# Kernel tuning notes

Measured on AMD Instinct MI355X. Metric: run time of the kernel, lower is better.

Reference implementation:

```python
import jax, jax.numpy as jnp
import numpy as np

N = 50000
E = 800000
G = 8
IN, HID, OUT = 128, 256, 128
BN_EPS = 1e-5


def _linear_params(key, fan_in, fan_out):
    k1, k2 = jax.random.split(key)
    s = 1.0 / np.sqrt(fan_in)
    w = jax.random.uniform(k1, (fan_out, fan_in), jnp.float32, -s, s)
    b = jax.random.uniform(k2, (fan_out,), jnp.float32, -s, s)
    return w, b


def setup_inputs() -> dict:
    key = jax.random.key(0)
    ks = jax.random.split(key, 16)
    inp = {
        "x": jax.random.normal(ks[0], (N, IN), jnp.float32),
        "src": jax.random.randint(ks[1], (E,), 0, N, jnp.int32),
        "dst": jax.random.randint(ks[2], (E,), 0, N, jnp.int32),
        "graph_ids": jnp.sort(jax.random.randint(ks[3], (N,), 0, G, jnp.int32)),
    }
    dims = [(IN, HID, HID), (HID, HID, HID), (HID, OUT, OUT)]
    for i, (d_in, d_mid, d_out) in enumerate(dims):
        kk = jax.random.split(ks[4 + i], 2)
        w1, b1 = _linear_params(kk[0], d_in, d_mid)
        w2, b2 = _linear_params(kk[1], d_mid, d_out)
        inp[f"w1_{i}"] = w1
        inp[f"b1_{i}"] = b1
        inp[f"w2_{i}"] = w2
        inp[f"b2_{i}"] = b2
        inp[f"eps_{i}"] = jnp.zeros((), jnp.float32)          # learn_eps, init 0
        inp[f"gamma_{i}"] = jnp.ones((d_out,), jnp.float32)   # BatchNorm weight
        inp[f"beta_{i}"] = jnp.zeros((d_out,), jnp.float32)   # BatchNorm bias
    return inp


def _gin_layer(h, src, dst, w1, b1, w2, b2, eps, gamma, beta):
    # GINConv: (1 + eps) * h_v + sum_{u in N(v)} h_u   (copy_u / sum)
    agg = jax.ops.segment_sum(h[src], dst, num_segments=N)
    z = (1.0 + eps) * h + agg
    # 2-layer MLP with ReLU
    z = jnp.maximum(z @ w1.T + b1, 0.0) @ w2.T + b2
    # BatchNorm1d (training-mode batch statistics, biased variance)
    mu = jnp.mean(z, axis=0)
    var = jnp.var(z, axis=0)
    return (z - mu) * jax.lax.rsqrt(var + BN_EPS) * gamma + beta


def reference(x, src, dst, graph_ids,
              w1_0, b1_0, w2_0, b2_0, eps_0, gamma_0, beta_0,
              w1_1, b1_1, w2_1, b2_1, eps_1, gamma_1, beta_1,
              w1_2, b1_2, w2_2, b2_2, eps_2, gamma_2, beta_2):
    h = _gin_layer(x, src, dst, w1_0, b1_0, w2_0, b2_0, eps_0, gamma_0, beta_0)
    h = jnp.maximum(h, 0.0)  # relu (dropout = identity in eval)
    h = _gin_layer(h, src, dst, w1_1, b1_1, w2_1, b2_1, eps_1, gamma_1, beta_1)
    h = jnp.maximum(h, 0.0)
    h = _gin_layer(h, src, dst, w1_2, b1_2, w2_2, b2_2, eps_2, gamma_2, beta_2)
    # dgl.mean_nodes: per-graph mean over nodes -> [G, OUT]
    sums = jax.ops.segment_sum(h, graph_ids, num_segments=G)
    counts = jax.ops.segment_sum(jnp.ones((N,), h.dtype), graph_ids, num_segments=G)
    return sums / jnp.maximum(counts, 1.0)[:, None]
```

## Files before the change

kernel.cpp:

```cpp
#include <hip/hip_runtime.h>

#define NG 8

typedef _Float16 half8  __attribute__((ext_vector_type(8)));
typedef float    f32x16 __attribute__((ext_vector_type(16)));


__global__ __launch_bounds__(256)
void k_cast16(const float* __restrict__ in, _Float16* __restrict__ out, int n8) {
    int i = blockIdx.x * 256 + threadIdx.x;
    if (i < n8) {
        const float4 a = *(const float4*)(in + (size_t)i * 8);
        const float4 b = *(const float4*)(in + (size_t)i * 8 + 4);
        half8 o;
        o[0] = (_Float16)a.x; o[1] = (_Float16)a.y; o[2] = (_Float16)a.z; o[3] = (_Float16)a.w;
        o[4] = (_Float16)b.x; o[5] = (_Float16)b.y; o[6] = (_Float16)b.z; o[7] = (_Float16)b.w;
        *(half8*)(out + (size_t)i * 8) = o;
    }
}

__global__ __launch_bounds__(256)
void k_castw(const float* __restrict__ w0, const float* __restrict__ w1,
             const float* __restrict__ w2, const float* __restrict__ w3,
             const float* __restrict__ w4, const float* __restrict__ w5,
             _Float16* __restrict__ o0, _Float16* __restrict__ o1,
             _Float16* __restrict__ o2, _Float16* __restrict__ o3,
             _Float16* __restrict__ o4, _Float16* __restrict__ o5) {
    int i = blockIdx.x * 256 + threadIdx.x;
    const float* in; _Float16* out; int off;
    if      (i <  4096) { in = w0; out = o0; off = 0;     }
    else if (i < 12288) { in = w1; out = o1; off = 4096;  }
    else if (i < 20480) { in = w2; out = o2; off = 12288; }
    else if (i < 28672) { in = w3; out = o3; off = 20480; }
    else if (i < 32768) { in = w4; out = o4; off = 28672; }
    else if (i < 34816) { in = w5; out = o5; off = 32768; }
    else return;
    int j = i - off;
    const float4 a = *(const float4*)(in + (size_t)j * 8);
    const float4 b = *(const float4*)(in + (size_t)j * 8 + 4);
    half8 o;
    o[0] = (_Float16)a.x; o[1] = (_Float16)a.y; o[2] = (_Float16)a.z; o[3] = (_Float16)a.w;
    o[4] = (_Float16)b.x; o[5] = (_Float16)b.y; o[6] = (_Float16)b.z; o[7] = (_Float16)b.w;
    *(half8*)(out + (size_t)j * 8) = o;
}


__global__ __launch_bounds__(256)
void k_deg(const int* __restrict__ dst, int* __restrict__ deg, int E) {
    int i = blockIdx.x * 256 + threadIdx.x;
    if (i < E) atomicAdd(&deg[dst[i]], 1);
}

__global__ __launch_bounds__(1024)
void k_scan_a(const int* __restrict__ deg, int* __restrict__ incl,
              int* __restrict__ bsum, int n) {
    __shared__ int s[1024];
    int t = threadIdx.x;
    int base = blockIdx.x * 1024;
    int v = (base + t < n) ? deg[base + t] : 0;
    s[t] = v;
    __syncthreads();
    for (int off = 1; off < 1024; off <<= 1) {
        int x = 0;
        if (t >= off) x = s[t - off];
        __syncthreads();
        if (t >= off) s[t] += x;
        __syncthreads();
    }
    if (base + t < n) incl[base + t] = s[t];
    if (t == 1023) bsum[blockIdx.x] = s[1023];
}

__global__ void k_scan_b(int* bsum, int nb) {
    if (threadIdx.x == 0 && blockIdx.x == 0) {
        int run = 0;
        for (int i = 0; i < nb; ++i) { int v = bsum[i]; bsum[i] = run; run += v; }
    }
}

__global__ __launch_bounds__(256)
void k_scan_c(const int* __restrict__ incl, const int* __restrict__ deg,
              const int* __restrict__ bsum, int* __restrict__ rowp, int n) {
    int i = blockIdx.x * 256 + threadIdx.x;
    if (i < n) rowp[i] = incl[i] - deg[i] + bsum[i >> 10];
}

__global__ __launch_bounds__(256)
void k_scatter(const int* __restrict__ src, const int* __restrict__ dst,
               const int* __restrict__ rowp, int* __restrict__ cur,
               int* __restrict__ ss, int E) {
    int i = blockIdx.x * 256 + threadIdx.x;
    if (i < E) {
        int d = dst[i];
        int pos = rowp[d] + atomicAdd(&cur[d], 1);
        ss[pos] = src[i];
    }
}


template<int K, bool AFFINE>
__global__ __launch_bounds__(256)
void k_agg16(const _Float16* __restrict__ h, const int* __restrict__ rowp,
             const int* __restrict__ deg, const int* __restrict__ ss,
             const float* __restrict__ eps, const float* __restrict__ scp,
             const float* __restrict__ shp, _Float16* __restrict__ z, int n) {
    constexpr int TPN = K / 8;
    constexpr int NPB = 256 / TPN;
    int node = blockIdx.x * NPB + threadIdx.x / TPN;
    int lane = threadIdx.x % TPN;
    if (node >= n) return;
    float e1 = 1.0f + eps[0];
    const int c0 = lane * 8;
    float sc[8], sh[8];
    if (AFFINE) {
#pragma unroll
        for (int e = 0; e < 8; ++e) { sc[e] = scp[c0 + e]; sh[e] = shp[c0 + e]; }
    }
    size_t base = (size_t)node * K + c0;
    half8 v = *(const half8*)(h + base);
    float a[8];
#pragma unroll
    for (int e = 0; e < 8; ++e) {
        float f = (float)v[e];
        if (AFFINE) f = fmaxf(f * sc[e] + sh[e], 0.0f);
        a[e] = f * e1;
    }
    int s  = rowp[node];
    int dn = deg[node];
    int j = 0;
    for (; j + 4 <= dn; j += 4) {
        int u0 = ss[s + j], u1 = ss[s + j + 1], u2 = ss[s + j + 2], u3 = ss[s + j + 3];
        half8 h0 = *(const half8*)(h + (size_t)u0 * K + c0);
        half8 h1 = *(const half8*)(h + (size_t)u1 * K + c0);
        half8 h2 = *(const half8*)(h + (size_t)u2 * K + c0);
        half8 h3 = *(const half8*)(h + (size_t)u3 * K + c0);
#pragma unroll
        for (int e = 0; e < 8; ++e) {
            float f0 = (float)h0[e], f1 = (float)h1[e];
            float f2 = (float)h2[e], f3 = (float)h3[e];
            if (AFFINE) {
                f0 = fmaxf(f0 * sc[e] + sh[e], 0.0f);
                f1 = fmaxf(f1 * sc[e] + sh[e], 0.0f);
                f2 = fmaxf(f2 * sc[e] + sh[e], 0.0f);
                f3 = fmaxf(f3 * sc[e] + sh[e], 0.0f);
            }
            a[e] += (f0 + f1) + (f2 + f3);
        }
    }
    for (; j < dn; ++j) {
        int u = ss[s + j];
        half8 hv = *(const half8*)(h + (size_t)u * K + c0);
#pragma unroll
        for (int e = 0; e < 8; ++e) {
            float f = (float)hv[e];
            if (AFFINE) f = fmaxf(f * sc[e] + sh[e], 0.0f);
            a[e] += f;
        }
    }
    half8 o;
#pragma unroll
    for (int e = 0; e < 8; ++e) o[e] = (_Float16)a[e];
    *(half8*)(z + base) = o;
}


template<int K, int MID, int MOUT>
__global__ __launch_bounds__(512)
void k_mlp3(const _Float16* __restrict__ A, const _Float16* __restrict__ W1,
            const float* __restrict__ b1, const _Float16* __restrict__ W2,
            const float* __restrict__ b2, _Float16* __restrict__ C,
            float* __restrict__ partial, int n, int ntiles) {
    constexpr int NK1 = K / 16;
    constexpr int NK2 = MID / 16;
    constexpr int MF1 = (MID == 256) ? 2 : 1;
    constexpr int MF2 = (MOUT == 256) ? 2 : 1;
    constexpr int NLD = K / 64;
    __shared__ char As[64 * 512];
    __shared__ char Ys[64 * 512];
    __shared__ char tbs[8 * 2304];
    const int tid  = threadIdx.x;
    const int lane = tid & 63;
    const int wid  = tid >> 6;
    const int lo   = lane & 31;
    const int hi   = lane >> 5;

    const int wc1 = (MID == 256) ? wid : (wid & 3);
    const int wr1 = (MID == 256) ? 0   : (wid >> 2);
    const int colbase1 = wc1 * 32;
    const int wc2 = (MOUT == 256) ? wid : (wid & 3);
    const int wr2 = (MOUT == 256) ? 0   : (wid >> 2);
    const int colbase2 = wc2 * 32;

    half8 w1f[NK1], w2f[NK2];
#pragma unroll
    for (int ks = 0; ks < NK1; ++ks)
        w1f[ks] = *(const half8*)(W1 + (size_t)(colbase1 + lo) * K + ks * 16 + hi * 8);
#pragma unroll
    for (int ks = 0; ks < NK2; ++ks)
        w2f[ks] = *(const half8*)(W2 + (size_t)(colbase2 + lo) * MID + ks * 16 + hi * 8);
    const float bb1 = b1[colbase1 + lo];
    const float bb2 = b2[colbase2 + lo];

    const int sr = tid >> 3;
    const int sl = tid & 7;
    const int g  = lane & 3;
    const int rl = lane >> 2;
    char* tb = tbs + wid * 2304;

    float s[8], q[8];
#pragma unroll
    for (int e = 0; e < 8; ++e) { s[e] = 0.f; q[e] = 0.f; }

    int tile = blockIdx.x;
    uint4 ar[NLD];
    if (tile < ntiles) {
        int ga = tile * 64 + sr; if (ga > n - 1) ga = n - 1;
        const char* Ab = (const char*)(A + (size_t)ga * K);
#pragma unroll
        for (int i = 0; i < NLD; ++i) ar[i] = *(const uint4*)(Ab + (sl + i * 8) * 16);
    }

    for (; tile < ntiles; tile += gridDim.x) {
        const int brow = tile * 64;

#pragma unroll
        for (int i = 0; i < NLD; ++i)
            *(uint4*)(As + sr * 512 + (((sl + i * 8) ^ (sr & 31)) << 4)) = ar[i];
        int nt = tile + gridDim.x;
        if (nt < ntiles) {
            int ga = nt * 64 + sr; if (ga > n - 1) ga = n - 1;
            const char* Ab = (const char*)(A + (size_t)ga * K);
#pragma unroll
            for (int i = 0; i < NLD; ++i) ar[i] = *(const uint4*)(Ab + (sl + i * 8) * 16);
        }
        __syncthreads();

        f32x16 acc1[MF1];
#pragma unroll
        for (int mf = 0; mf < MF1; ++mf)
#pragma unroll
            for (int e = 0; e < 16; ++e) acc1[mf][e] = 0.0f;
#pragma unroll
        for (int ks = 0; ks < NK1; ++ks) {
#pragma unroll
            for (int mf = 0; mf < MF1; ++mf) {
                int r = ((wr1 + mf) << 5) + lo;
                half8 af = *(const half8*)(As + r * 512 + ((ks * 32 + hi * 16) ^ ((r & 31) << 4)));
                acc1[mf] = __builtin_amdgcn_mfma_f32_32x32x16_f16(af, w1f[ks], acc1[mf], 0, 0, 0);
            }
        }
#pragma unroll
        for (int mf = 0; mf < MF1; ++mf) {
            int rb = ((wr1 + mf) << 5) + (hi << 2);
#pragma unroll
            for (int j = 0; j < 16; ++j) {
                int r = rb + (j & 3) + ((j >> 2) << 3);
                float v = fmaxf(acc1[mf][j] + bb1, 0.0f);
                *(_Float16*)(Ys + r * 512 + (((colbase1 + lo) * 2) ^ ((r & 31) << 4))) = (_Float16)v;
            }
        }
        __syncthreads();

        f32x16 acc2[MF2];
#pragma unroll
        for (int mf = 0; mf < MF2; ++mf)
#pragma unroll
            for (int e = 0; e < 16; ++e) acc2[mf][e] = 0.0f;
#pragma unroll
        for (int ks = 0; ks < NK2; ++ks) {
#pragma unroll
            for (int mf = 0; mf < MF2; ++mf) {
                int r = ((wr2 + mf) << 5) + lo;
                half8 af = *(const half8*)(Ys + r * 512 + ((ks * 32 + hi * 16) ^ ((r & 31) << 4)));
                acc2[mf] = __builtin_amdgcn_mfma_f32_32x32x16_f16(af, w2f[ks], acc2[mf], 0, 0, 0);
            }
        }

#pragma unroll
        for (int mf = 0; mf < MF2; ++mf) {
#pragma unroll
            for (int j = 0; j < 16; ++j) {
                int tr = (j & 3) + ((j >> 2) << 3) + (hi << 2);
                *(_Float16*)(tb + tr * 72 + lo * 2) = (_Float16)(acc2[mf][j] + bb2);
            }
#pragma unroll
            for (int it = 0; it < 2; ++it) {
                int lr = it * 16 + rl;
                int grow = brow + ((wr2 + mf) << 5) + lr;
                half8 v = *(const half8*)(tb + lr * 72 + g * 16);
                if (grow < n) {
                    *(half8*)(C + (size_t)grow * MOUT + colbase2 + g * 8) = v;
#pragma unroll
                    for (int e = 0; e < 8; ++e) { float f = (float)v[e]; s[e] += f; q[e] += f * f; }
                }
            }
        }
    }

#pragma unroll
    for (int e = 0; e < 8; ++e) {
        for (int mk = 4; mk < 64; mk <<= 1) {
            s[e] += __shfl_xor(s[e], mk, 64);
            q[e] += __shfl_xor(q[e], mk, 64);
        }
    }
    if (lane < 4) {
        float* p = partial + ((size_t)blockIdx.x * 2 + wr2) * (2 * MOUT);
#pragma unroll
        for (int e = 0; e < 8; ++e) {
            p[colbase2 + lane * 8 + e]        = s[e];
            p[MOUT + colbase2 + lane * 8 + e] = q[e];
        }
    }
}


template<int M>
__global__ __launch_bounds__(256)
void k_bnred(const float* __restrict__ partial, const float* __restrict__ gamma,
             const float* __restrict__ beta, float* __restrict__ scale,
             float* __restrict__ shift, int n, int count, int step) {
    const int w = threadIdx.x >> 6, lane = threadIdx.x & 63;
    const int c = blockIdx.x * 4 + w;
    float s = 0.f, q = 0.f;
    for (int b = lane; b < count; b += 64) {
        const float* p = partial + (size_t)(b * step) * (2 * M);
        s += p[c];
        q += p[M + c];
    }
#pragma unroll
    for (int mk = 1; mk < 64; mk <<= 1) {
        s += __shfl_xor(s, mk, 64);
        q += __shfl_xor(q, mk, 64);
    }
    if (lane == 0) {
        float invN = 1.0f / (float)n;
        float mean = s * invN;
        float var  = q * invN - mean * mean;
        float sc   = rsqrtf(var + 1e-5f) * gamma[c];
        scale[c] = sc;
        shift[c] = beta[c] - mean * sc;
    }
}


__global__ __launch_bounds__(256)
void k_readout_bn(const _Float16* __restrict__ z, const float* __restrict__ scale,
                  const float* __restrict__ shift, const int* __restrict__ gid,
                  float* __restrict__ gsum, int* __restrict__ gcnt, int n) {
    __shared__ float ls[NG * 128];
    __shared__ int   lc[NG];
    for (int i = threadIdx.x; i < NG * 128; i += 256) ls[i] = 0.0f;
    if (threadIdx.x < NG) lc[threadIdx.x] = 0;
    __syncthreads();
    int c  = threadIdx.x & 127;
    int ro = threadIdx.x >> 7;
    const float sc = scale[c];
    const float sh = shift[c];
    for (int r = blockIdx.x * 2 + ro; r < n; r += gridDim.x * 2) {
        int g = gid[r];
        float v = (float)z[(size_t)r * 128 + c] * sc + sh;
        atomicAdd(&ls[g * 128 + c], v);
        if (c == 0) atomicAdd(&lc[g], 1);
    }
    __syncthreads();
    for (int i = threadIdx.x; i < NG * 128; i += 256) atomicAdd(&gsum[i], ls[i]);
    if (threadIdx.x < NG) atomicAdd(&gcnt[threadIdx.x], lc[threadIdx.x]);
}

__global__ void k_final(const float* __restrict__ gsum, const int* __restrict__ gcnt,
                        float* __restrict__ out) {
    int i = blockIdx.x * 256 + threadIdx.x;
    if (i < NG * 128) {
        int g = i >> 7;
        out[i] = gsum[i] / fmaxf((float)gcnt[g], 1.0f);
    }
}


extern "C" void kernel_launch(void* const* d_in, const int* in_sizes, int n_in,
                              void* d_out, int out_size, void* d_ws, size_t ws_size,
                              hipStream_t stream) {
    const float* x   = (const float*)d_in[0];
    const int*   src = (const int*)d_in[1];
    const int*   dst = (const int*)d_in[2];
    const int*   gid = (const int*)d_in[3];
    const int n = in_sizes[0] / 128;
    const int E = in_sizes[1];

    auto align = [](size_t o) { return (o + 255) & ~(size_t)255; };
    char* ws = (char*)d_ws;
    size_t off = 0;
    const size_t SZ_H = align((size_t)n * 256 * sizeof(_Float16));
    const size_t SZ_I = align((size_t)n * sizeof(int));
    const int gx = (n + 63) / 64;
    const int NBLK = 256;

    _Float16* h0 = (_Float16*)(ws + off); off += align((size_t)n * 128 * sizeof(_Float16));
    _Float16* P0 = (_Float16*)(ws + off); off += SZ_H;
    _Float16* P1 = (_Float16*)(ws + off); off += SZ_H;
    int*   deg  = (int*)(ws + off);   off += SZ_I;
    int*   incl = (int*)(ws + off);   off += SZ_I;
    int*   rowp = (int*)(ws + off);   off += SZ_I;
    int*   cur  = (int*)(ws + off);   off += SZ_I;
    int*   bsum = (int*)(ws + off);   off += 256 * sizeof(int);
    int*   ss   = (int*)(ws + off);   off += align((size_t)E * sizeof(int));
    float* partial = (float*)(ws + off); off += align((size_t)(2 * NBLK) * 2 * 256 * sizeof(float));
    float* scale   = (float*)(ws + off); off += align(256 * sizeof(float));
    float* shiftb  = (float*)(ws + off); off += align(256 * sizeof(float));
    float* gsum = (float*)(ws + off); off += align(NG * 128 * sizeof(float));
    int*   gcnt = (int*)(ws + off);   off += align(NG * sizeof(int));
    _Float16* wh[6];
    for (int i = 0; i < 6; ++i) { wh[i] = (_Float16*)(ws + off); off += align(65536 * sizeof(_Float16)); }

    k_cast16<<<(n * 128 / 8 + 255) / 256, 256, 0, stream>>>(x, h0, n * 128 / 8);
    k_castw<<<136, 256, 0, stream>>>(
        (const float*)d_in[4], (const float*)d_in[6],
        (const float*)d_in[11], (const float*)d_in[13],
        (const float*)d_in[18], (const float*)d_in[20],
        wh[0], wh[1], wh[2], wh[3], wh[4], wh[5]);

    hipMemsetAsync(deg, 0, (size_t)n * sizeof(int), stream);
    k_deg<<<(E + 255) / 256, 256, 0, stream>>>(dst, deg, E);
    int nb = (n + 1023) / 1024;
    k_scan_a<<<nb, 1024, 0, stream>>>(deg, incl, bsum, n);
    k_scan_b<<<1, 1, 0, stream>>>(bsum, nb);
    k_scan_c<<<(n + 255) / 256, 256, 0, stream>>>(incl, deg, bsum, rowp, n);
    hipMemsetAsync(cur, 0, (size_t)n * sizeof(int), stream);
    k_scatter<<<(E + 255) / 256, 256, 0, stream>>>(src, dst, rowp, cur, ss, E);

    for (int L = 0; L < 3; ++L) {
        const int base = 4 + 7 * L;
        const float* b1    = (const float*)d_in[base + 1];
        const float* b2    = (const float*)d_in[base + 3];
        const float* eps   = (const float*)d_in[base + 4];
        const float* gamma = (const float*)d_in[base + 5];
        const float* beta  = (const float*)d_in[base + 6];

        if (L == 0) {
            k_agg16<128, false><<<(n + 15) / 16, 256, 0, stream>>>(
                h0, rowp, deg, ss, eps, nullptr, nullptr, P1, n);
            k_mlp3<128, 256, 256><<<NBLK, 512, 0, stream>>>(P1, wh[0], b1, wh[1], b2, P0, partial, n, gx);
            k_bnred<256><<<64, 256, 0, stream>>>(partial, gamma, beta, scale, shiftb, n, NBLK, 2);
        } else if (L == 1) {
            k_agg16<256, true><<<(n + 7) / 8, 256, 0, stream>>>(
                P0, rowp, deg, ss, eps, scale, shiftb, P1, n);
            k_mlp3<256, 256, 256><<<NBLK, 512, 0, stream>>>(P1, wh[2], b1, wh[3], b2, P0, partial, n, gx);
            k_bnred<256><<<64, 256, 0, stream>>>(partial, gamma, beta, scale, shiftb, n, NBLK, 2);
        } else {
            k_agg16<256, true><<<(n + 7) / 8, 256, 0, stream>>>(
                P0, rowp, deg, ss, eps, scale, shiftb, P1, n);
            k_mlp3<256, 128, 128><<<NBLK, 512, 0, stream>>>(P1, wh[4], b1, wh[5], b2, P0, partial, n, gx);
            k_bnred<128><<<32, 256, 0, stream>>>(partial, gamma, beta, scale, shiftb, n, 2 * NBLK, 1);
        }
    }

    hipMemsetAsync(gsum, 0, NG * 128 * sizeof(float), stream);
    hipMemsetAsync(gcnt, 0, NG * sizeof(int), stream);
    k_readout_bn<<<256, 256, 0, stream>>>(P0, scale, shiftb, gid, gsum, gcnt, n);
    k_final<<<4, 256, 0, stream>>>(gsum, gcnt, (float*)d_out);
}
```

Before: 411.5 us.

## Transpose fp16 weight layout for coalesced fragment loads; accumulate readout per graph run

The weight cast kernel now writes weights in a k-slot-major layout, so each lane's 8-half fragment load in the fused MLP kernel hits contiguous addresses across lanes instead of strided rows. The readout kernel keeps a register accumulator while the sorted graph id stays the same and only issues shared-memory atomics when the graph changes, rather than one atomic per row. The weight layout change couples the cast kernel and the MLP kernel. The readout change depends on graph_ids being sorted to pay off.

```diff
diff --git a/kernel.cpp b/kernel.cpp
--- a/kernel.cpp
+++ b/kernel.cpp
@@ -27,17 +27,20 @@
              _Float16* __restrict__ o2, _Float16* __restrict__ o3,
              _Float16* __restrict__ o4, _Float16* __restrict__ o5) {
     int i = blockIdx.x * 256 + threadIdx.x;
-    const float* in; _Float16* out; int off;
-    if      (i <  4096) { in = w0; out = o0; off = 0;     }
-    else if (i < 12288) { in = w1; out = o1; off = 4096;  }
-    else if (i < 20480) { in = w2; out = o2; off = 12288; }
-    else if (i < 28672) { in = w3; out = o3; off = 20480; }
-    else if (i < 32768) { in = w4; out = o4; off = 28672; }
-    else if (i < 34816) { in = w5; out = o5; off = 32768; }
+    const float* in; _Float16* out; int off, lgC, K;
+    if      (i <  4096) { in = w0; out = o0; off = 0;     lgC = 8; K = 128; }
+    else if (i < 12288) { in = w1; out = o1; off = 4096;  lgC = 8; K = 256; }
+    else if (i < 20480) { in = w2; out = o2; off = 12288; lgC = 8; K = 256; }
+    else if (i < 28672) { in = w3; out = o3; off = 20480; lgC = 8; K = 256; }
+    else if (i < 32768) { in = w4; out = o4; off = 28672; lgC = 7; K = 256; }
+    else if (i < 34816) { in = w5; out = o5; off = 32768; lgC = 7; K = 128; }
     else return;
     int j = i - off;
-    const float4 a = *(const float4*)(in + (size_t)j * 8);
-    const float4 b = *(const float4*)(in + (size_t)j * 8 + 4);
+    int kslot = j >> lgC;
+    int c = j & ((1 << lgC) - 1);
+    const float* s = in + (size_t)c * K + kslot * 8;
+    const float4 a = *(const float4*)(s);
+    const float4 b = *(const float4*)(s + 4);
     half8 o;
     o[0] = (_Float16)a.x; o[1] = (_Float16)a.y; o[2] = (_Float16)a.z; o[3] = (_Float16)a.w;
     o[4] = (_Float16)b.x; o[5] = (_Float16)b.y; o[6] = (_Float16)b.z; o[7] = (_Float16)b.w;
@@ -194,10 +197,10 @@
     half8 w1f[NK1], w2f[NK2];
 #pragma unroll
     for (int ks = 0; ks < NK1; ++ks)
-        w1f[ks] = *(const half8*)(W1 + (size_t)(colbase1 + lo) * K + ks * 16 + hi * 8);
+        w1f[ks] = *(const half8*)(W1 + ((size_t)(ks * 2 + hi) * MID + colbase1 + lo) * 8);
 #pragma unroll
     for (int ks = 0; ks < NK2; ++ks)
-        w2f[ks] = *(const half8*)(W2 + (size_t)(colbase2 + lo) * MID + ks * 16 + hi * 8);
+        w2f[ks] = *(const half8*)(W2 + ((size_t)(ks * 2 + hi) * MOUT + colbase2 + lo) * 8);
     const float bb1 = b1[colbase1 + lo];
     const float bb2 = b2[colbase2 + lo];
 
@@ -357,11 +360,23 @@
     int ro = threadIdx.x >> 7;
     const float sc = scale[c];
     const float sh = shift[c];
+    float acc = 0.0f;
+    int cnt = 0, curg = -1;
     for (int r = blockIdx.x * 2 + ro; r < n; r += gridDim.x * 2) {
         int g = gid[r];
-        float v = (float)z[(size_t)r * 128 + c] * sc + sh;
-        atomicAdd(&ls[g * 128 + c], v);
-        if (c == 0) atomicAdd(&lc[g], 1);
+        if (g != curg) {
+            if (curg >= 0) {
+                atomicAdd(&ls[curg * 128 + c], acc);
+                if (c == 0) atomicAdd(&lc[curg], cnt);
+            }
+            curg = g; acc = 0.0f; cnt = 0;
+        }
+        acc += (float)z[(size_t)r * 128 + c] * sc + sh;
+        ++cnt;
+    }
+    if (curg >= 0) {
+        atomicAdd(&ls[curg * 128 + c], acc);
+        if (c == 0) atomicAdd(&lc[curg], cnt);
     }
     __syncthreads();
     for (int i = threadIdx.x; i < NG * 128; i += 256) atomicAdd(&gsum[i], ls[i]);
```

Measured after the change: 416.4 us. No clear change (+1.2%).
